# Performance work log

Measured on AMD Instinct MI355X. Metric: run time of the kernel, lower is better.

Reference implementation:

```python
import jax, jax.numpy as jnp
import numpy as np

N, E, G = 50000, 800000, 128
IN, HID, HEAD = 1280, 256, 4
DH = HID // HEAD
EPS = 1e-5
ATT_SCALE = 1.0 / np.sqrt(1280.0).astype(np.float32)  # hardcoded in source


def _seg_softmax(x, seg, n):
    # softmax over segments along axis 0; x: [K] or [K, H]
    m = jax.ops.segment_max(x, seg, num_segments=n)
    e = jnp.exp(x - m[seg])
    s = jax.ops.segment_sum(e, seg, num_segments=n)
    return e / s[seg]


def _bn(x, g, b):
    # eval-mode BatchNorm1d with init running stats (mean=0, var=1)
    return g * x * (1.0 / np.sqrt(1.0 + EPS)) + b


def _ln(x, g, b):
    mu = x.mean(-1, keepdims=True)
    var = ((x - mu) ** 2).mean(-1, keepdims=True)
    return g * (x - mu) / jnp.sqrt(var + EPS) + b


def setup_inputs() -> dict:
    key = jax.random.key(0)
    ks = jax.random.split(key, 40)
    rn = lambda i, shp, s=0.05: jax.random.normal(ks[i], shp, jnp.float32) * s
    inp = {
        "h": jax.random.normal(ks[0], (N, IN), jnp.float32),
        "gcn_w0": rn(1, (IN, HID)), "gcn_b0": rn(2, (HID,), 0.01),
        "gcn_w1": rn(3, (HID, HID)), "gcn_b1": rn(4, (HID,), 0.01),
        "bn_gcn0_g": 1.0 + rn(5, (HID,), 0.1), "bn_gcn0_b": rn(6, (HID,), 0.01),
        "bn_gcn1_g": 1.0 + rn(7, (HID,), 0.1), "bn_gcn1_b": rn(8, (HID,), 0.01),
        "gat_w0": rn(9, (IN, HID)), "gat_al0": rn(10, (HEAD, DH)), "gat_ar0": rn(11, (HEAD, DH)), "gat_bias0": rn(12, (HID,), 0.01),
        "gat_w1": rn(13, (HID, HID)), "gat_al1": rn(14, (HEAD, DH)), "gat_ar1": rn(15, (HEAD, DH)), "gat_bias1": rn(16, (HID,), 0.01),
        "bn_gat0_g": 1.0 + rn(17, (HID,), 0.1), "bn_gat0_b": rn(18, (HID,), 0.01),
        "bn_gat1_g": 1.0 + rn(19, (HID,), 0.1), "bn_gat1_b": rn(20, (HID,), 0.01),
        "gate_w": rn(21, (2 * HID, HID)), "gate_b": rn(22, (HID,), 0.01),
        "qw": rn(23, (HEAD, HID, HID)), "kw": rn(24, (HEAD, HID, HID)), "vw": rn(25, (HEAD, HID, HID)),
        "ct_w": rn(26, (HEAD * HID, HID)),
        "ff_w1": rn(27, (HID, 2 * HID)), "ff_b1": rn(28, (2 * HID,), 0.01),
        "ff_w2": rn(29, (2 * HID, HID)), "ff_b2": rn(30, (HID,), 0.01),
        "ln_g": 1.0 + rn(31, (HID,), 0.1), "ln_b": rn(32, (HID,), 0.01),
        "src": jax.random.randint(ks[33], (E,), 0, N, jnp.int32),
        "dst": jax.random.randint(ks[34], (E,), 0, N, jnp.int32),
        "gid": jnp.sort(jax.random.randint(ks[35], (N,), 0, G, jnp.int32)),
        "num_graphs": G,
    }
    return inp


def reference(h, gcn_w0, gcn_b0, gcn_w1, gcn_b1, bn_gcn0_g, bn_gcn0_b, bn_gcn1_g, bn_gcn1_b,
              gat_w0, gat_al0, gat_ar0, gat_bias0, gat_w1, gat_al1, gat_ar1, gat_bias1,
              bn_gat0_g, bn_gat0_b, bn_gat1_g, bn_gat1_b, gate_w, gate_b,
              qw, kw, vw, ct_w, ff_w1, ff_b1, ff_w2, ff_b2, ln_g, ln_b,
              src, dst, gid, num_graphs):
    n = h.shape[0]
    ones_e = jnp.ones(src.shape[0], h.dtype)
    # dgl.mean_nodes per graph
    cnt = jnp.clip(jax.ops.segment_sum(jnp.ones(n, h.dtype), gid, num_segments=num_graphs), 1.0)
    init_avg_h = jax.ops.segment_sum(h, gid, num_segments=num_graphs) / cnt[:, None]
    # GraphConv norm='both', degrees clamped to >=1
    deg_out = jnp.clip(jax.ops.segment_sum(ones_e, src, num_segments=n), 1.0)
    deg_in = jnp.clip(jax.ops.segment_sum(ones_e, dst, num_segments=n), 1.0)
    ns, nd = deg_out ** -0.5, deg_in ** -0.5

    def gcn(x, w, b):
        m = (x * ns[:, None]) @ w  # [N, HID]
        return jax.ops.segment_sum(m[src], dst, num_segments=n) * nd[:, None] + b

    hg = jax.nn.relu(_bn(gcn(h, gcn_w0, gcn_b0), bn_gcn0_g, bn_gcn0_b))
    hg = jax.nn.relu(_bn(gcn(hg, gcn_w1, gcn_b1), bn_gcn1_g, bn_gcn1_b)) + hg

    def gat(x, w, al, ar, b):
        f = (x @ w).reshape(n, HEAD, DH)
        el = (f * al).sum(-1)  # [N, HEAD]
        er = (f * ar).sum(-1)
        e = jax.nn.leaky_relu(el[src] + er[dst], 0.2)  # [E, HEAD]
        alpha = _seg_softmax(e, dst, n)  # edge softmax over incoming edges
        out = jax.ops.segment_sum(alpha[:, :, None] * f[src], dst, num_segments=n)
        return out.reshape(n, HID) + b

    ha = jax.nn.elu(_bn(gat(h, gat_w0, gat_al0, gat_ar0, gat_bias0), bn_gat0_g, bn_gat0_b))
    ha = jax.nn.elu(_bn(gat(ha, gat_w1, gat_al1, gat_ar1, gat_bias1), bn_gat1_g, bn_gat1_b)) + ha

    gate = jax.nn.sigmoid(jnp.concatenate([hg, ha], axis=1) @ gate_w + gate_b)
    x = gate * hg + (1.0 - gate) * ha  # residue_h

    # transformer_block: per-graph node softmax attention
    q = jnp.einsum('nd,hde->nhe', x, qw)
    k = jnp.einsum('nd,hde->nhe', x, kw)
    v = jnp.einsum('nd,hde->nhe', x, vw)
    att = (q * k).sum(-1) * ATT_SCALE  # [N, HEAD]
    alpha = _seg_softmax(att, gid, num_graphs)  # dgl.softmax_nodes per head
    mo = (v * alpha[:, :, None]).reshape(n, HEAD * HID) @ ct_w
    x1 = _ln(mo + x, ln_g, ln_b)
    x2 = _ln(jax.nn.relu(x1 @ ff_w1 + ff_b1) @ ff_w2 + ff_b2 + x1, ln_g, ln_b)

    readout = jax.ops.segment_sum(x2, gid, num_segments=num_graphs)
    return readout, init_avg_h
```

## Files before the change

### kernel.cpp

```cpp
#include <hip/hip_runtime.h>

#define NN 50000
#define NE 800000
#define NG 128
#define DIN 1280
#define HIDDEN 256
#define BNS 0.9999950000374997f
#define ATT_SCALE 0.027950849718747373f
#define LN_EPS 1e-5f

typedef __attribute__((ext_vector_type(8))) short short8;
typedef __attribute__((ext_vector_type(4))) float floatx4;

__device__ __forceinline__ float b2f(unsigned short u) {
  return __uint_as_float(((unsigned int)u) << 16);
}
__device__ __forceinline__ unsigned short f2b(float f) {
  unsigned int x = __float_as_uint(f);
  x += 0x7fffu + ((x >> 16) & 1u);
  return (unsigned short)(x >> 16);
}

__global__ void transpose_w_k(const float* __restrict__ src, unsigned short* __restrict__ dst,
                              int K, int Nc) {
  int idx = blockIdx.x * 256 + threadIdx.x;
  if (idx >= K * Nc) return;
  int n = idx / K, k = idx % K;
  dst[idx] = f2b(src[(size_t)k * Nc + n]);
}

__global__ void mw_k(const float* __restrict__ qw, const float* __restrict__ kw,
                     unsigned short* __restrict__ dst) {
  int col = blockIdx.x;
  int d = threadIdx.x;
  int hh = col >> 8, dp = col & 255;
  const float* qr = qw + ((size_t)hh * 256 + d) * 256;
  const float* kr = kw + ((size_t)hh * 256 + dp) * 256;
  float s = 0.f;
  for (int e = 0; e < 256; e += 4) {
    float4 a = *(const float4*)(qr + e);
    float4 b = *(const float4*)(kr + e);
    s += a.x * b.x + a.y * b.y + a.z * b.z + a.w * b.w;
  }
  dst[(size_t)col * 256 + d] = f2b(s);
}

__global__ void w2_k(const float* __restrict__ vw, const float* __restrict__ ctw,
                     unsigned short* __restrict__ dst) {
  int b = blockIdx.x;
  int c = threadIdx.x;
  int hh = b >> 8, d = b & 255;
  const float* vr = vw + ((size_t)hh * 256 + d) * 256;
  float s = 0.f;
  for (int e = 0; e < 256; ++e)
    s += vr[e] * ctw[(size_t)(hh * 256 + e) * 256 + c];
  dst[(size_t)c * 1024 + b] = f2b(s);
}

__global__ void cvt_avg_k(const float* __restrict__ h, const int* __restrict__ gid,
                          unsigned short* __restrict__ h_bf, float* __restrict__ out1) {
  int row0 = blockIdx.x * 50;
  int tid = threadIdx.x;
  float acc[5] = {0, 0, 0, 0, 0};
  int cur_g = gid[row0];
  for (int r = 0; r < 50; ++r) {
    int row = row0 + r;
    int g = gid[row];
    if (g != cur_g) {
#pragma unroll
      for (int j = 0; j < 5; ++j) {
        atomicAdd(&out1[(size_t)cur_g * DIN + j * 256 + tid], acc[j]);
        acc[j] = 0.f;
      }
      cur_g = g;
    }
#pragma unroll
    for (int j = 0; j < 5; ++j) {
      float v = h[(size_t)row * DIN + j * 256 + tid];
      acc[j] += v;
      h_bf[(size_t)row * DIN + j * 256 + tid] = f2b(v);
    }
  }
#pragma unroll
  for (int j = 0; j < 5; ++j)
    atomicAdd(&out1[(size_t)cur_g * DIN + j * 256 + tid], acc[j]);
}

__global__ void div_avg_k(const int* __restrict__ start, float* __restrict__ out1) {
  int idx = blockIdx.x * 256 + threadIdx.x;
  if (idx >= NG * DIN) return;
  int g = idx / DIN;
  float cnt = (float)(start[g + 1] - start[g]);
  if (cnt < 1.f) cnt = 1.f;
  out1[idx] /= cnt;
}

__global__ void graph_bounds_k(const int* __restrict__ gid, int* __restrict__ start, int n) {
  int i = blockIdx.x * 256 + threadIdx.x;
  if (i >= n) return;
  int g = gid[i];
  if (i == 0) {
    for (int gg = 0; gg <= g; ++gg) start[gg] = 0;
  } else {
    int gp = gid[i - 1];
    for (int gg = gp + 1; gg <= g; ++gg) start[gg] = i;
  }
  if (i == n - 1) {
    for (int gg = g + 1; gg <= NG; ++gg) start[gg] = n;
  }
}

__global__ void degrees_k(const int* __restrict__ src, const int* __restrict__ dst,
                          int* __restrict__ deg_out, int* __restrict__ deg_in, int e) {
  int i = blockIdx.x * 256 + threadIdx.x;
  if (i >= e) return;
  atomicAdd(&deg_out[src[i]], 1);
  atomicAdd(&deg_in[dst[i]], 1);
}

__global__ void invsqrt_k(const int* __restrict__ deg_out, const int* __restrict__ deg_in,
                          float* __restrict__ ns, float* __restrict__ nd, int n) {
  int i = blockIdx.x * 256 + threadIdx.x;
  if (i >= n) return;
  int a = deg_out[i]; if (a < 1) a = 1;
  int b = deg_in[i];  if (b < 1) b = 1;
  ns[i] = rsqrtf((float)a);
  nd[i] = rsqrtf((float)b);
}

__global__ void scan_local_k(const int* __restrict__ deg, int* __restrict__ row_ptr,
                             int* __restrict__ bsum) {
  __shared__ int buf[256];
  int b = blockIdx.x, t = threadIdx.x;
  int i = b * 256 + t;
  int v = (i < NN) ? deg[i] : 0;
  buf[t] = v;
  __syncthreads();
  for (int off = 1; off < 256; off <<= 1) {
    int tv = (t >= off) ? buf[t - off] : 0;
    __syncthreads();
    buf[t] += tv;
    __syncthreads();
  }
  if (i < NN) row_ptr[i] = buf[t] - v;
  if (t == 255) bsum[b] = buf[255];
}

__global__ void scan_bsum_k(int* __restrict__ bsum, int* __restrict__ boff, int nb,
                            int* __restrict__ row_ptr) {
  __shared__ int buf[256];
  int t = threadIdx.x;
  int v = (t < nb) ? bsum[t] : 0;
  buf[t] = v;
  __syncthreads();
  for (int off = 1; off < 256; off <<= 1) {
    int tv = (t >= off) ? buf[t - off] : 0;
    __syncthreads();
    buf[t] += tv;
    __syncthreads();
  }
  if (t < nb) boff[t] = buf[t] - v;
  if (t == 0) row_ptr[NN] = NE;
}

__global__ void scan_add_k(int* __restrict__ row_ptr, const int* __restrict__ boff) {
  int i = blockIdx.x * 256 + threadIdx.x;
  if (i >= NN) return;
  row_ptr[i] += boff[blockIdx.x];
}

__global__ void fill_csr_k(const int* __restrict__ src, const int* __restrict__ dst,
                           const int* __restrict__ row_ptr, int* __restrict__ fill,
                           int* __restrict__ csr_src, int e) {
  int i = blockIdx.x * 256 + threadIdx.x;
  if (i >= e) return;
  int d = dst[i];
  int pos = row_ptr[d] + atomicAdd(&fill[d], 1);
  csr_src[pos] = src[i];
}

template <int MODE>
__global__ __launch_bounds__(256, 2) void gemm_bf16(const unsigned short* __restrict__ A,
                                                    const unsigned short* __restrict__ Bt,
                                                    void* __restrict__ Cout,
                                                    const float* __restrict__ bias,
                                                    int M, int K, int Nc,
                                                    const unsigned short* __restrict__ xtile,
                                                    float* __restrict__ attp,
                                                    const float* __restrict__ ascale) {
  __shared__ unsigned short sbuf[16384];
  unsigned short* lA = sbuf;
  unsigned short* lB = sbuf + 8192;
  const int tid = threadIdx.x;
  const int n0 = blockIdx.x * 128;
  const int m0 = blockIdx.y * 128;
  const int w = tid >> 6;
  const int lane = tid & 63;
  const int wr = (w >> 1) * 64;
  const int wc = (w & 1) * 64;
  const int quad = lane >> 4;
  const int l15 = lane & 15;
  const int js = tid & 7;
  const int mbase = tid >> 3;
  const int wbase = w * 64;

  floatx4 acc[4][4];
#pragma unroll
  for (int i = 0; i < 4; ++i)
#pragma unroll
    for (int j = 0; j < 4; ++j) acc[i][j] = (floatx4)0.0f;

  for (int k0 = 0; k0 < K; k0 += 64) {
    __syncthreads();
    if (MODE == 6) {
#pragma unroll
      for (int it = 0; it < 4; ++it) {
        int m = it * 32 + mbase;
        int gm = m0 + m;
        if (gm >= M) gm = M - 1;
        uint4 va = *(const uint4*)(A + (size_t)gm * 256 + (k0 & 255) + js * 8);
        float s = ascale[(size_t)gm * 4 + (k0 >> 8)];
        unsigned short* pp = (unsigned short*)&va;
#pragma unroll
        for (int c = 0; c < 8; ++c) pp[c] = f2b(b2f(pp[c]) * s);
        *(uint4*)(lA + (size_t)(m * 8 + (js ^ (m & 7))) * 8) = va;
      }
    } else {
#pragma unroll
      for (int it = 0; it < 4; ++it) {
        int c = it * 256 + wbase + lane;
        int m = c >> 3, g = c & 7;
        int gm = m0 + m;
        if (gm >= M) gm = M - 1;
        const unsigned short* gp = A + (size_t)gm * K + k0 + (g ^ (m & 7)) * 8;
        __builtin_amdgcn_global_load_lds(
            (const __attribute__((address_space(1))) unsigned int*)gp,
            (__attribute__((address_space(3))) unsigned int*)(lA + (size_t)(it * 256 + wbase) * 8),
            16, 0, 0);
      }
    }
#pragma unroll
    for (int it = 0; it < 4; ++it) {
      int c = it * 256 + wbase + lane;
      int m = c >> 3, g = c & 7;
      int gn = n0 + m;
      const unsigned short* gp = Bt + (size_t)gn * K + k0 + (g ^ (m & 7)) * 8;
      __builtin_amdgcn_global_load_lds(
          (const __attribute__((address_space(1))) unsigned int*)gp,
          (__attribute__((address_space(3))) unsigned int*)(lB + (size_t)(it * 256 + wbase) * 8),
          16, 0, 0);
    }
    __syncthreads();
#pragma unroll
    for (int ks = 0; ks < 2; ++ks) {
      int kb = ks * 4 + quad;
      short8 af[4], bfr[4];
#pragma unroll
      for (int ri = 0; ri < 4; ++ri) {
        int r = wr + ri * 16 + l15;
        af[ri] = *(const short8*)(lA + (size_t)(r * 8 + (kb ^ (r & 7))) * 8);
      }
#pragma unroll
      for (int ci = 0; ci < 4; ++ci) {
        int c = wc + ci * 16 + l15;
        bfr[ci] = *(const short8*)(lB + (size_t)(c * 8 + (kb ^ (c & 7))) * 8);
      }
#pragma unroll
      for (int ri = 0; ri < 4; ++ri)
#pragma unroll
        for (int ci = 0; ci < 4; ++ci)
          acc[ri][ci] = __builtin_amdgcn_mfma_f32_16x16x32_bf16(af[ri], bfr[ci], acc[ri][ci], 0, 0, 0);
    }
  }

  if (MODE == 4) {
    __syncthreads();
    int cb = n0 & 255;
#pragma unroll
    for (int it2 = 0; it2 < 8; ++it2) {
      int linear = it2 * 256 + tid;
      int rr = linear >> 4;
      int c8 = (linear & 15) * 8;
      int gr = m0 + rr;
      if (gr >= M) gr = M - 1;
      *(uint4*)(sbuf + rr * 128 + c8) = *(const uint4*)(xtile + (size_t)gr * 256 + cb + c8);
    }
    __syncthreads();
    int head = n0 >> 8;
#pragma unroll
    for (int ri = 0; ri < 4; ++ri) {
      int lrow = wr + ri * 16 + quad * 4;
#pragma unroll
      for (int r = 0; r < 4; ++r) {
        float p = 0.f;
#pragma unroll
        for (int ci = 0; ci < 4; ++ci)
          p += acc[ri][ci][r] * b2f(sbuf[(lrow + r) * 128 + wc + ci * 16 + l15]);
        p += __shfl_xor(p, 1);
        p += __shfl_xor(p, 2);
        p += __shfl_xor(p, 4);
        p += __shfl_xor(p, 8);
        if (l15 == 0) {
          int grow = m0 + lrow + r;
          if (grow < M) atomicAdd(&attp[(size_t)grow * 4 + head], p * ATT_SCALE);
        }
      }
    }
    return;
  }

  if (MODE == 7) {
#pragma unroll
    for (int ri = 0; ri < 4; ++ri) {
      int row = m0 + wr + ri * 16 + quad * 4;
#pragma unroll
      for (int ci = 0; ci < 4; ++ci) {
        int col = n0 + wc + ci * 16 + l15;
        float bv = bias[col];
#pragma unroll
        for (int r = 0; r < 4; ++r) {
          if (row + r < M) {
            float g = 1.f / (1.f + expf(-(acc[ri][ci][r] + bv)));
            float hg = b2f(xtile[(size_t)(row + r) * 512 + col]);
            float ha = b2f(xtile[(size_t)(row + r) * 512 + 256 + col]);
            ((unsigned short*)Cout)[(size_t)(row + r) * Nc + col] = f2b(g * hg + (1.f - g) * ha);
          }
        }
      }
    }
    return;
  }

#pragma unroll
  for (int ri = 0; ri < 4; ++ri) {
    int row = m0 + wr + ri * 16 + quad * 4;
#pragma unroll
    for (int ci = 0; ci < 4; ++ci) {
      int col = n0 + wc + ci * 16 + l15;
      float bv = (MODE == 2) ? bias[col] : 0.f;
#pragma unroll
      for (int r = 0; r < 4; ++r) {
        if (row + r < M) {
          float v = acc[ri][ci][r];
          if (MODE == 2) { v += bv; v = fmaxf(v, 0.f); }
          if (MODE == 1)
            ((float*)Cout)[(size_t)(row + r) * Nc + col] = v;
          else
            ((unsigned short*)Cout)[(size_t)(row + r) * Nc + col] = f2b(v);
        }
      }
    }
  }
}

__global__ void gcn_agg_k(const unsigned short* __restrict__ m, int ldm,
                          const int* __restrict__ row_ptr, const int* __restrict__ csr_src,
                          const float* __restrict__ ns, const float* __restrict__ nd,
                          const float* __restrict__ bias,
                          const float* __restrict__ bng, const float* __restrict__ bnb,
                          const unsigned short* __restrict__ resid, int ldr,
                          unsigned short* __restrict__ out, int ldo) {
  int node = blockIdx.x * 4 + (threadIdx.x >> 6);
  if (node >= NN) return;
  int lane = threadIdx.x & 63;
  int s = row_ptr[node], e = row_ptr[node + 1];
  float a0 = 0, a1 = 0, a2 = 0, a3 = 0;
  for (int i = s; i < e; ++i) {
    int u = csr_src[i];
    float w = ns[u];
    ushort4 v = *(const ushort4*)(m + (size_t)u * ldm + lane * 4);
    a0 += w * b2f(v.x); a1 += w * b2f(v.y); a2 += w * b2f(v.z); a3 += w * b2f(v.w);
  }
  float ndv = nd[node];
  int col = lane * 4;
  float vals[4] = {a0, a1, a2, a3};
  ushort4 o;
#pragma unroll
  for (int c = 0; c < 4; ++c) {
    float v = vals[c] * ndv + bias[col + c];
    v = bng[col + c] * v * BNS + bnb[col + c];
    v = fmaxf(v, 0.f);
    if (resid) v += b2f(resid[(size_t)node * ldr + col + c]);
    ((unsigned short*)&o)[c] = f2b(v);
  }
  *(ushort4*)(out + (size_t)node * ldo + col) = o;
}

__global__ void elr_k(const unsigned short* __restrict__ f, int ldf,
                      const float* __restrict__ al, const float* __restrict__ ar,
                      float* __restrict__ elr) {
  int node = blockIdx.x * 4 + (threadIdx.x >> 6);
  if (node >= NN) return;
  int lane = threadIdx.x & 63;
  int head = lane >> 4;
  int col = lane * 4;
  int dcol = col & 63;
  ushort4 v = *(const ushort4*)(f + (size_t)node * ldf + col);
  float pl = 0, pr = 0;
#pragma unroll
  for (int c = 0; c < 4; ++c) {
    float x = b2f(((unsigned short*)&v)[c]);
    pl += x * al[head * 64 + dcol + c];
    pr += x * ar[head * 64 + dcol + c];
  }
#pragma unroll
  for (int off = 1; off < 16; off <<= 1) {
    pl += __shfl_xor(pl, off);
    pr += __shfl_xor(pr, off);
  }
  if ((lane & 15) == 0) {
    elr[(size_t)node * 8 + head] = pl;
    elr[(size_t)node * 8 + 4 + head] = pr;
  }
}

__global__ void gat_agg_k(const unsigned short* __restrict__ f, int ldf,
                          const int* __restrict__ row_ptr, const int* __restrict__ csr_src,
                          const float* __restrict__ elr,
                          const float* __restrict__ bias,
                          const float* __restrict__ bng, const float* __restrict__ bnb,
                          const unsigned short* __restrict__ resid, int ldr,
                          unsigned short* __restrict__ out, int ldo) {
  int node = blockIdx.x * 4 + (threadIdx.x >> 6);
  if (node >= NN) return;
  int lane = threadIdx.x & 63;
  int s = row_ptr[node], e = row_ptr[node + 1];
  float4 er = *(const float4*)(elr + (size_t)node * 8 + 4);
  float m0 = -1e30f, m1 = -1e30f, m2 = -1e30f, m3 = -1e30f;
  for (int i = s + lane; i < e; i += 64) {
    int u = csr_src[i];
    float4 el = *(const float4*)(elr + (size_t)u * 8);
    float t;
    t = el.x + er.x; t = t > 0.f ? t : 0.2f * t; m0 = fmaxf(m0, t);
    t = el.y + er.y; t = t > 0.f ? t : 0.2f * t; m1 = fmaxf(m1, t);
    t = el.z + er.z; t = t > 0.f ? t : 0.2f * t; m2 = fmaxf(m2, t);
    t = el.w + er.w; t = t > 0.f ? t : 0.2f * t; m3 = fmaxf(m3, t);
  }
#pragma unroll
  for (int off = 1; off < 64; off <<= 1) {
    m0 = fmaxf(m0, __shfl_xor(m0, off));
    m1 = fmaxf(m1, __shfl_xor(m1, off));
    m2 = fmaxf(m2, __shfl_xor(m2, off));
    m3 = fmaxf(m3, __shfl_xor(m3, off));
  }
  float s0 = 0, s1 = 0, s2 = 0, s3 = 0;
  for (int i = s + lane; i < e; i += 64) {
    int u = csr_src[i];
    float4 el = *(const float4*)(elr + (size_t)u * 8);
    float t;
    t = el.x + er.x; t = t > 0.f ? t : 0.2f * t; s0 += expf(t - m0);
    t = el.y + er.y; t = t > 0.f ? t : 0.2f * t; s1 += expf(t - m1);
    t = el.z + er.z; t = t > 0.f ? t : 0.2f * t; s2 += expf(t - m2);
    t = el.w + er.w; t = t > 0.f ? t : 0.2f * t; s3 += expf(t - m3);
  }
#pragma unroll
  for (int off = 1; off < 64; off <<= 1) {
    s0 += __shfl_xor(s0, off);
    s1 += __shfl_xor(s1, off);
    s2 += __shfl_xor(s2, off);
    s3 += __shfl_xor(s3, off);
  }
  int head = lane >> 4;
  float erh = head == 0 ? er.x : head == 1 ? er.y : head == 2 ? er.z : er.w;
  float mh = head == 0 ? m0 : head == 1 ? m1 : head == 2 ? m2 : m3;
  float sh = head == 0 ? s0 : head == 1 ? s1 : head == 2 ? s2 : s3;
  float inv_sh = (sh > 0.f) ? 1.f / sh : 0.f;
  float a0 = 0, a1 = 0, a2 = 0, a3 = 0;
  for (int i = s; i < e; ++i) {
    int u = csr_src[i];
    float t = elr[(size_t)u * 8 + head] + erh;
    t = t > 0.f ? t : 0.2f * t;
    float wgt = expf(t - mh) * inv_sh;
    ushort4 v = *(const ushort4*)(f + (size_t)u * ldf + lane * 4);
    a0 += wgt * b2f(v.x); a1 += wgt * b2f(v.y); a2 += wgt * b2f(v.z); a3 += wgt * b2f(v.w);
  }
  int col = lane * 4;
  float vals[4] = {a0, a1, a2, a3};
  ushort4 o;
#pragma unroll
  for (int c = 0; c < 4; ++c) {
    float v = vals[c] + bias[col + c];
    v = bng[col + c] * v * BNS + bnb[col + c];
    v = (v > 0.f) ? v : (expf(v) - 1.f);
    if (resid) v += b2f(resid[(size_t)node * ldr + col + c]);
    ((unsigned short*)&o)[c] = f2b(v);
  }
  *(ushort4*)(out + (size_t)node * ldo + col) = o;
}

__global__ void gsoftmax_k(const float* __restrict__ att, const int* __restrict__ start,
                           float* __restrict__ alpha) {
  int g = blockIdx.x;
  int s = start[g], e = start[g + 1];
  int tid = threadIdx.x;
  __shared__ float red[256];
  __shared__ float mh[4], sh[4];
  float lm[4] = {-1e30f, -1e30f, -1e30f, -1e30f};
  for (int i = s + tid; i < e; i += 256) {
    float4 a = *(const float4*)(att + (size_t)i * 4);
    lm[0] = fmaxf(lm[0], a.x); lm[1] = fmaxf(lm[1], a.y);
    lm[2] = fmaxf(lm[2], a.z); lm[3] = fmaxf(lm[3], a.w);
  }
#pragma unroll
  for (int h = 0; h < 4; ++h) {
    red[tid] = lm[h]; __syncthreads();
    for (int off = 128; off > 0; off >>= 1) {
      if (tid < off) red[tid] = fmaxf(red[tid], red[tid + off]);
      __syncthreads();
    }
    if (tid == 0) mh[h] = red[0];
    __syncthreads();
  }
  float ls[4] = {0, 0, 0, 0};
  for (int i = s + tid; i < e; i += 256) {
    float4 a = *(const float4*)(att + (size_t)i * 4);
    ls[0] += expf(a.x - mh[0]); ls[1] += expf(a.y - mh[1]);
    ls[2] += expf(a.z - mh[2]); ls[3] += expf(a.w - mh[3]);
  }
#pragma unroll
  for (int h = 0; h < 4; ++h) {
    red[tid] = ls[h]; __syncthreads();
    for (int off = 128; off > 0; off >>= 1) {
      if (tid < off) red[tid] += red[tid + off];
      __syncthreads();
    }
    if (tid == 0) sh[h] = red[0];
    __syncthreads();
  }
  for (int i = s + tid; i < e; i += 256) {
    float4 a = *(const float4*)(att + (size_t)i * 4);
    float4 o;
    o.x = expf(a.x - mh[0]) / sh[0];
    o.y = expf(a.y - mh[1]) / sh[1];
    o.z = expf(a.z - mh[2]) / sh[2];
    o.w = expf(a.w - mh[3]) / sh[3];
    *(float4*)(alpha + (size_t)i * 4) = o;
  }
}

__global__ void ln1_k(const unsigned short* __restrict__ mo, const unsigned short* __restrict__ x,
                      const float* __restrict__ g, const float* __restrict__ b,
                      unsigned short* __restrict__ x1) {
  int node = blockIdx.x * 4 + (threadIdx.x >> 6);
  if (node >= NN) return;
  int lane = threadIdx.x & 63;
  int c = lane * 4;
  ushort4 a = *(const ushort4*)(mo + (size_t)node * HIDDEN + c);
  ushort4 xx = *(const ushort4*)(x + (size_t)node * HIDDEN + c);
  float v0 = b2f(a.x) + b2f(xx.x), v1 = b2f(a.y) + b2f(xx.y);
  float v2 = b2f(a.z) + b2f(xx.z), v3 = b2f(a.w) + b2f(xx.w);
  float sm = v0 + v1 + v2 + v3;
#pragma unroll
  for (int off = 1; off < 64; off <<= 1) sm += __shfl_xor(sm, off);
  float mu = sm * (1.f / 256.f);
  float d0 = v0 - mu, d1 = v1 - mu, d2 = v2 - mu, d3 = v3 - mu;
  float sq = d0 * d0 + d1 * d1 + d2 * d2 + d3 * d3;
#pragma unroll
  for (int off = 1; off < 64; off <<= 1) sq += __shfl_xor(sq, off);
  float inv = rsqrtf(sq * (1.f / 256.f) + LN_EPS);
  ushort4 ob;
  ob.x = f2b(g[c + 0] * d0 * inv + b[c + 0]);
  ob.y = f2b(g[c + 1] * d1 * inv + b[c + 1]);
  ob.z = f2b(g[c + 2] * d2 * inv + b[c + 2]);
  ob.w = f2b(g[c + 3] * d3 * inv + b[c + 3]);
  *(ushort4*)(x1 + (size_t)node * HIDDEN + c) = ob;
}

__global__ void ln2_k(const unsigned short* __restrict__ ff2o, const float* __restrict__ ffb2,
                      const unsigned short* __restrict__ x1,
                      const float* __restrict__ g, const float* __restrict__ b,
                      unsigned short* __restrict__ x2) {
  int node = blockIdx.x * 4 + (threadIdx.x >> 6);
  if (node >= NN) return;
  int lane = threadIdx.x & 63;
  int c = lane * 4;
  ushort4 a = *(const ushort4*)(ff2o + (size_t)node * HIDDEN + c);
  ushort4 xx = *(const ushort4*)(x1 + (size_t)node * HIDDEN + c);
  float v0 = b2f(a.x) + ffb2[c + 0] + b2f(xx.x), v1 = b2f(a.y) + ffb2[c + 1] + b2f(xx.y);
  float v2 = b2f(a.z) + ffb2[c + 2] + b2f(xx.z), v3 = b2f(a.w) + ffb2[c + 3] + b2f(xx.w);
  float sm = v0 + v1 + v2 + v3;
#pragma unroll
  for (int off = 1; off < 64; off <<= 1) sm += __shfl_xor(sm, off);
  float mu = sm * (1.f / 256.f);
  float d0 = v0 - mu, d1 = v1 - mu, d2 = v2 - mu, d3 = v3 - mu;
  float sq = d0 * d0 + d1 * d1 + d2 * d2 + d3 * d3;
#pragma unroll
  for (int off = 1; off < 64; off <<= 1) sq += __shfl_xor(sq, off);
  float inv = rsqrtf(sq * (1.f / 256.f) + LN_EPS);
  ushort4 ob;
  ob.x = f2b(g[c + 0] * d0 * inv + b[c + 0]);
  ob.y = f2b(g[c + 1] * d1 * inv + b[c + 1]);
  ob.z = f2b(g[c + 2] * d2 * inv + b[c + 2]);
  ob.w = f2b(g[c + 3] * d3 * inv + b[c + 3]);
  *(ushort4*)(x2 + (size_t)node * HIDDEN + c) = ob;
}

__global__ void readout_k(const unsigned short* __restrict__ x2, const int* __restrict__ start,
                          float* __restrict__ out0) {
  int g = blockIdx.x;
  int c = threadIdx.x;
  float acc = 0.f;
  for (int i = start[g]; i < start[g + 1]; ++i) acc += b2f(x2[(size_t)i * HIDDEN + c]);
  out0[(size_t)g * HIDDEN + c] = acc;
}

static const size_t OFF_BUFA   = 0;
static const size_t OFF_C01    = 128000000;
static const size_t OFF_HG0    = 179200000;
static const size_t OFF_HA0    = 204800000;
static const size_t OFF_M1     = 230400000;
static const size_t OFF_F1     = 256000000;
static const size_t OFF_XCAT   = 281600000;
static const size_t OFF_GLOGIT = 332800000;
static const size_t OFF_XB     = 358400000;
static const size_t OFF_MO     = 384000000;
static const size_t OFF_X1     = 409600000;
static const size_t OFF_ATT    = 435200000;
static const size_t OFF_ALPHA  = OFF_ATT + 800000;
static const size_t OFF_ELR0   = OFF_ALPHA + 800000;
static const size_t OFF_ELR1   = OFF_ELR0 + 1600000;
static const size_t OFF_START  = OFF_ELR1 + 1600000;
static const size_t OFF_DEGO   = OFF_START + 1024;
static const size_t OFF_DEGI   = OFF_DEGO + 200704;
static const size_t OFF_NS     = OFF_DEGI + 200704;
static const size_t OFF_ND     = OFF_NS + 200704;
static const size_t OFF_ROWP   = OFF_ND + 200704;
static const size_t OFF_FILL   = OFF_ROWP + 200704;
static const size_t OFF_BSUM   = OFF_FILL + 200704;
static const size_t OFF_BOFF   = OFF_BSUM + 1024;
static const size_t OFF_CSRS   = OFF_BOFF + 1024;
static const size_t OFF_W01T   = OFF_CSRS + 3200000;
static const size_t OFF_W1T    = OFF_W01T + 1310720;
static const size_t OFF_W1GT   = OFF_W1T + 131072;
static const size_t OFF_GATEWT = OFF_W1GT + 131072;
static const size_t OFF_WMVT   = OFF_GATEWT + 262144;
static const size_t OFF_CTWT   = OFF_WMVT + 1048576;
static const size_t OFF_FFW1T  = OFF_CTWT + 524288;
static const size_t OFF_FFW2T  = OFF_FFW1T + 262144;
static const size_t WS_NEED    = OFF_FFW2T + 262144;

extern "C" void kernel_launch(void* const* d_in, const int* in_sizes, int n_in,
                              void* d_out, int out_size, void* d_ws, size_t ws_size,
                              hipStream_t stream) {
  if (ws_size < WS_NEED) return;

  const float* h       = (const float*)d_in[0];
  const float* gcn_w0  = (const float*)d_in[1];
  const float* gcn_b0  = (const float*)d_in[2];
  const float* gcn_w1  = (const float*)d_in[3];
  const float* gcn_b1  = (const float*)d_in[4];
  const float* bn_gcn0_g = (const float*)d_in[5];
  const float* bn_gcn0_b = (const float*)d_in[6];
  const float* bn_gcn1_g = (const float*)d_in[7];
  const float* bn_gcn1_b = (const float*)d_in[8];
  const float* gat_w0  = (const float*)d_in[9];
  const float* gat_al0 = (const float*)d_in[10];
  const float* gat_ar0 = (const float*)d_in[11];
  const float* gat_bias0 = (const float*)d_in[12];
  const float* gat_w1  = (const float*)d_in[13];
  const float* gat_al1 = (const float*)d_in[14];
  const float* gat_ar1 = (const float*)d_in[15];
  const float* gat_bias1 = (const float*)d_in[16];
  const float* bn_gat0_g = (const float*)d_in[17];
  const float* bn_gat0_b = (const float*)d_in[18];
  const float* bn_gat1_g = (const float*)d_in[19];
  const float* bn_gat1_b = (const float*)d_in[20];
  const float* gate_w  = (const float*)d_in[21];
  const float* gate_b  = (const float*)d_in[22];
  const float* qw      = (const float*)d_in[23];
  const float* kw      = (const float*)d_in[24];
  const float* vw      = (const float*)d_in[25];
  const float* ct_w    = (const float*)d_in[26];
  const float* ff_w1   = (const float*)d_in[27];
  const float* ff_b1   = (const float*)d_in[28];
  const float* ff_w2   = (const float*)d_in[29];
  const float* ff_b2   = (const float*)d_in[30];
  const float* ln_g    = (const float*)d_in[31];
  const float* ln_b    = (const float*)d_in[32];
  const int* srcv = (const int*)d_in[33];
  const int* dstv = (const int*)d_in[34];
  const int* gid  = (const int*)d_in[35];

  char* ws = (char*)d_ws;
  unsigned short* h_bf = (unsigned short*)(ws + OFF_BUFA);
  unsigned short* ff1o = (unsigned short*)(ws + OFF_BUFA);
  unsigned short* ff2o = (unsigned short*)(ws + OFF_BUFA + 51200000);
  unsigned short* x2   = (unsigned short*)(ws + OFF_BUFA + 76800000);
  unsigned short* c01  = (unsigned short*)(ws + OFF_C01);
  unsigned short* hg0  = (unsigned short*)(ws + OFF_HG0);
  unsigned short* ha0  = (unsigned short*)(ws + OFF_HA0);
  unsigned short* m1   = (unsigned short*)(ws + OFF_M1);
  unsigned short* f1   = (unsigned short*)(ws + OFF_F1);
  unsigned short* xcat = (unsigned short*)(ws + OFF_XCAT);
  unsigned short* xb   = (unsigned short*)(ws + OFF_XB);
  unsigned short* mo   = (unsigned short*)(ws + OFF_MO);
  unsigned short* x1   = (unsigned short*)(ws + OFF_X1);
  float* att           = (float*)(ws + OFF_ATT);
  float* alpha         = (float*)(ws + OFF_ALPHA);
  float* elr0          = (float*)(ws + OFF_ELR0);
  float* elr1          = (float*)(ws + OFF_ELR1);
  int* start   = (int*)(ws + OFF_START);
  int* deg_out = (int*)(ws + OFF_DEGO);
  int* deg_in  = (int*)(ws + OFF_DEGI);
  float* ns    = (float*)(ws + OFF_NS);
  float* nd    = (float*)(ws + OFF_ND);
  int* row_ptr = (int*)(ws + OFF_ROWP);
  int* fill    = (int*)(ws + OFF_FILL);
  int* bsum    = (int*)(ws + OFF_BSUM);
  int* boff    = (int*)(ws + OFF_BOFF);
  int* csr_src = (int*)(ws + OFF_CSRS);
  unsigned short* w01t   = (unsigned short*)(ws + OFF_W01T);
  unsigned short* w1t    = (unsigned short*)(ws + OFF_W1T);
  unsigned short* w1gt   = (unsigned short*)(ws + OFF_W1GT);
  unsigned short* gatewt = (unsigned short*)(ws + OFF_GATEWT);
  unsigned short* wmvt   = (unsigned short*)(ws + OFF_WMVT);
  unsigned short* w2t    = (unsigned short*)(ws + OFF_CTWT);
  unsigned short* ffw1t  = (unsigned short*)(ws + OFF_FFW1T);
  unsigned short* ffw2t  = (unsigned short*)(ws + OFF_FFW2T);

  float* out0 = (float*)d_out;
  float* out1 = out0 + NG * HIDDEN;

  hipMemsetAsync(deg_out, 0, NN * 4, stream);
  hipMemsetAsync(deg_in, 0, NN * 4, stream);
  hipMemsetAsync(fill, 0, NN * 4, stream);
  hipMemsetAsync(out1, 0, NG * DIN * 4, stream);
  hipMemsetAsync(att, 0, NN * 4 * 4, stream);

  transpose_w_k<<<(1280 * 256 + 255) / 256, 256, 0, stream>>>(gcn_w0, w01t, 1280, 256);
  transpose_w_k<<<(1280 * 256 + 255) / 256, 256, 0, stream>>>(gat_w0, w01t + 256 * 1280, 1280, 256);
  transpose_w_k<<<(256 * 256 + 255) / 256, 256, 0, stream>>>(gcn_w1, w1t, 256, 256);
  transpose_w_k<<<(256 * 256 + 255) / 256, 256, 0, stream>>>(gat_w1, w1gt, 256, 256);
  transpose_w_k<<<(512 * 256 + 255) / 256, 256, 0, stream>>>(gate_w, gatewt, 512, 256);
  mw_k<<<1024, 256, 0, stream>>>(qw, kw, wmvt);
  w2_k<<<1024, 256, 0, stream>>>(vw, ct_w, w2t);
  transpose_w_k<<<(256 * 512 + 255) / 256, 256, 0, stream>>>(ff_w1, ffw1t, 256, 512);
  transpose_w_k<<<(512 * 256 + 255) / 256, 256, 0, stream>>>(ff_w2, ffw2t, 512, 256);

  graph_bounds_k<<<(NN + 255) / 256, 256, 0, stream>>>(gid, start, NN);
  degrees_k<<<(NE + 255) / 256, 256, 0, stream>>>(srcv, dstv, deg_out, deg_in, NE);
  invsqrt_k<<<(NN + 255) / 256, 256, 0, stream>>>(deg_out, deg_in, ns, nd, NN);
  const int NB_SCAN = (NN + 255) / 256;
  scan_local_k<<<NB_SCAN, 256, 0, stream>>>(deg_in, row_ptr, bsum);
  scan_bsum_k<<<1, 256, 0, stream>>>(bsum, boff, NB_SCAN, row_ptr);
  scan_add_k<<<NB_SCAN, 256, 0, stream>>>(row_ptr, boff);
  fill_csr_k<<<(NE + 255) / 256, 256, 0, stream>>>(srcv, dstv, row_ptr, fill, csr_src, NE);

  cvt_avg_k<<<NN / 50, 256, 0, stream>>>(h, gid, h_bf, out1);
  div_avg_k<<<(NG * DIN + 255) / 256, 256, 0, stream>>>(start, out1);

  const int MB = (NN + 127) / 128;
  gemm_bf16<0><<<dim3(4, MB), 256, 0, stream>>>(h_bf, w01t, c01, nullptr, NN, 1280, 512,
                                                nullptr, nullptr, nullptr);
  gcn_agg_k<<<NN / 4, 256, 0, stream>>>(c01, 512, row_ptr, csr_src, ns, nd,
                                        gcn_b0, bn_gcn0_g, bn_gcn0_b, nullptr, 0, hg0, 256);
  elr_k<<<NN / 4, 256, 0, stream>>>(c01 + 256, 512, gat_al0, gat_ar0, elr0);
  gat_agg_k<<<NN / 4, 256, 0, stream>>>(c01 + 256, 512, row_ptr, csr_src, elr0,
                                        gat_bias0, bn_gat0_g, bn_gat0_b, nullptr, 0, ha0, 256);
  gemm_bf16<0><<<dim3(2, MB), 256, 0, stream>>>(hg0, w1t, m1, nullptr, NN, 256, 256,
                                                nullptr, nullptr, nullptr);
  gcn_agg_k<<<NN / 4, 256, 0, stream>>>(m1, 256, row_ptr, csr_src, ns, nd,
                                        gcn_b1, bn_gcn1_g, bn_gcn1_b, hg0, 256, xcat, 512);
  gemm_bf16<0><<<dim3(2, MB), 256, 0, stream>>>(ha0, w1gt, f1, nullptr, NN, 256, 256,
                                                nullptr, nullptr, nullptr);
  elr_k<<<NN / 4, 256, 0, stream>>>(f1, 256, gat_al1, gat_ar1, elr1);
  gat_agg_k<<<NN / 4, 256, 0, stream>>>(f1, 256, row_ptr, csr_src, elr1,
                                        gat_bias1, bn_gat1_g, bn_gat1_b, ha0, 256, xcat + 256, 512);
  gemm_bf16<7><<<dim3(2, MB), 256, 0, stream>>>(xcat, gatewt, xb, gate_b, NN, 512, 256,
                                                xcat, nullptr, nullptr);
  gemm_bf16<4><<<dim3(8, MB), 256, 0, stream>>>(xb, wmvt, nullptr, nullptr, NN, 256, 1024,
                                                xb, att, nullptr);
  gsoftmax_k<<<NG, 256, 0, stream>>>(att, start, alpha);
  gemm_bf16<6><<<dim3(2, MB), 256, 0, stream>>>(xb, w2t, mo, nullptr, NN, 1024, 256,
                                                nullptr, nullptr, alpha);
  ln1_k<<<NN / 4, 256, 0, stream>>>(mo, xb, ln_g, ln_b, x1);
  gemm_bf16<2><<<dim3(4, MB), 256, 0, stream>>>(x1, ffw1t, ff1o, ff_b1, NN, 256, 512,
                                                nullptr, nullptr, nullptr);
  gemm_bf16<0><<<dim3(2, MB), 256, 0, stream>>>(ff1o, ffw2t, ff2o, nullptr, NN, 512, 256,
                                                nullptr, nullptr, nullptr);
  ln2_k<<<NN / 4, 256, 0, stream>>>(ff2o, ff_b2, x1, ln_g, ln_b, x2);
  readout_k<<<NG, 256, 0, stream>>>(x2, start, out0);
}
```

Measured before the change: 1.664 ms.

## Double-buffer GEMM LDS, fuse GAT el/er into GEMM, batch layer-1 GEMMs, fuse readout

The GEMM main loop now double-buffers its LDS tiles so the next K-tile's global-to-LDS loads overlap the current MFMA work. GAT attention logits (el/er) are computed in the GEMM epilogue, which removes the separate elr kernels. The two layer-1 GEMMs are batched into one launch using gridDim.z with fixed pointer offsets. The readout is fused into ln2 through per-node atomics, and cvt_avg is vectorised to float4 loads. LDS use doubles to 64KB per block, which may cut occupancy, and the per-node atomics into 128 graphs could contend.

Measured after the change: 1.830 ms. +9.9%, slower.

```diff
diff --git a/kernel.cpp b/kernel.cpp
--- a/kernel.cpp
+++ b/kernel.cpp
@@ -61,29 +61,30 @@
                           unsigned short* __restrict__ h_bf, float* __restrict__ out1) {
   int row0 = blockIdx.x * 50;
   int tid = threadIdx.x;
-  float acc[5] = {0, 0, 0, 0, 0};
+  float4 acc = {0.f, 0.f, 0.f, 0.f};
   int cur_g = gid[row0];
+  int c4 = tid * 4;
   for (int r = 0; r < 50; ++r) {
     int row = row0 + r;
     int g = gid[row];
     if (g != cur_g) {
-#pragma unroll
-      for (int j = 0; j < 5; ++j) {
-        atomicAdd(&out1[(size_t)cur_g * DIN + j * 256 + tid], acc[j]);
-        acc[j] = 0.f;
-      }
+      atomicAdd(&out1[(size_t)cur_g * DIN + c4 + 0], acc.x);
+      atomicAdd(&out1[(size_t)cur_g * DIN + c4 + 1], acc.y);
+      atomicAdd(&out1[(size_t)cur_g * DIN + c4 + 2], acc.z);
+      atomicAdd(&out1[(size_t)cur_g * DIN + c4 + 3], acc.w);
+      acc = {0.f, 0.f, 0.f, 0.f};
       cur_g = g;
     }
-#pragma unroll
-    for (int j = 0; j < 5; ++j) {
-      float v = h[(size_t)row * DIN + j * 256 + tid];
-      acc[j] += v;
-      h_bf[(size_t)row * DIN + j * 256 + tid] = f2b(v);
-    }
-  }
-#pragma unroll
-  for (int j = 0; j < 5; ++j)
-    atomicAdd(&out1[(size_t)cur_g * DIN + j * 256 + tid], acc[j]);
+    float4 v = *(const float4*)(h + (size_t)row * DIN + c4);
+    acc.x += v.x; acc.y += v.y; acc.z += v.z; acc.w += v.w;
+    ushort4 o;
+    o.x = f2b(v.x); o.y = f2b(v.y); o.z = f2b(v.z); o.w = f2b(v.w);
+    *(ushort4*)(h_bf + (size_t)row * DIN + c4) = o;
+  }
+  atomicAdd(&out1[(size_t)cur_g * DIN + c4 + 0], acc.x);
+  atomicAdd(&out1[(size_t)cur_g * DIN + c4 + 1], acc.y);
+  atomicAdd(&out1[(size_t)cur_g * DIN + c4 + 2], acc.z);
+  atomicAdd(&out1[(size_t)cur_g * DIN + c4 + 3], acc.w);
 }
 
 __global__ void div_avg_k(const int* __restrict__ start, float* __restrict__ out1) {
@@ -187,10 +188,12 @@
                                                     int M, int K, int Nc,
                                                     const unsigned short* __restrict__ xtile,
                                                     float* __restrict__ attp,
-                                                    const float* __restrict__ ascale) {
-  __shared__ unsigned short sbuf[16384];
-  unsigned short* lA = sbuf;
-  unsigned short* lB = sbuf + 8192;
+                                                    const float* __restrict__ ascale,
+                                                    const float* __restrict__ al,
+                                                    const float* __restrict__ ar,
+                                                    float* __restrict__ elr,
+                                                    int ecol0) {
+  __shared__ unsigned short sbuf[32768];
   const int tid = threadIdx.x;
   const int n0 = blockIdx.x * 128;
   const int m0 = blockIdx.y * 128;
@@ -204,77 +207,138 @@
   const int mbase = tid >> 3;
   const int wbase = w * 64;
 
+  bool do_elr = (MODE == 8);
+  const unsigned short* Ap = A;
+  const unsigned short* Bp = Bt;
+  unsigned short* Cp = (unsigned short*)Cout;
+  if (MODE == 8 && gridDim.z == 2) {
+    if (blockIdx.z == 0) {
+      do_elr = false;
+    } else {
+      Ap += 12800000;
+      Bp += 65536;
+      Cp += 12800000;
+    }
+  }
+
   floatx4 acc[4][4];
 #pragma unroll
   for (int i = 0; i < 4; ++i)
 #pragma unroll
     for (int j = 0; j < 4; ++j) acc[i][j] = (floatx4)0.0f;
 
-  for (int k0 = 0; k0 < K; k0 += 64) {
-    __syncthreads();
-    if (MODE == 6) {
+  if constexpr (MODE == 6) {
+    unsigned short* lA = sbuf;
+    unsigned short* lB = sbuf + 8192;
+    for (int k0 = 0; k0 < K; k0 += 64) {
+      __syncthreads();
 #pragma unroll
       for (int it = 0; it < 4; ++it) {
         int m = it * 32 + mbase;
         int gm = m0 + m;
         if (gm >= M) gm = M - 1;
-        uint4 va = *(const uint4*)(A + (size_t)gm * 256 + (k0 & 255) + js * 8);
+        uint4 va = *(const uint4*)(Ap + (size_t)gm * 256 + (k0 & 255) + js * 8);
         float s = ascale[(size_t)gm * 4 + (k0 >> 8)];
         unsigned short* pp = (unsigned short*)&va;
 #pragma unroll
         for (int c = 0; c < 8; ++c) pp[c] = f2b(b2f(pp[c]) * s);
         *(uint4*)(lA + (size_t)(m * 8 + (js ^ (m & 7))) * 8) = va;
       }
-    } else {
+#pragma unroll
+      for (int it = 0; it < 4; ++it) {
+        int c = it * 256 + wbase + lane;
+        int m = c >> 3, g = c & 7;
+        int gn = n0 + m;
+        const unsigned short* gp = Bp + (size_t)gn * K + k0 + (g ^ (m & 7)) * 8;
+        __builtin_amdgcn_global_load_lds(
+            (const __attribute__((address_space(1))) unsigned int*)gp,
+            (__attribute__((address_space(3))) unsigned int*)(lB + (size_t)(it * 256 + wbase) * 8),
+            16, 0, 0);
+      }
+      __syncthreads();
+#pragma unroll
+      for (int ks = 0; ks < 2; ++ks) {
+        int kb = ks * 4 + quad;
+        short8 af[4], bfr[4];
+#pragma unroll
+        for (int ri = 0; ri < 4; ++ri) {
+          int r = wr + ri * 16 + l15;
+          af[ri] = *(const short8*)(lA + (size_t)(r * 8 + (kb ^ (r & 7))) * 8);
+        }
+#pragma unroll
+        for (int ci = 0; ci < 4; ++ci) {
+          int c = wc + ci * 16 + l15;
+          bfr[ci] = *(const short8*)(lB + (size_t)(c * 8 + (kb ^ (c & 7))) * 8);
+        }
+#pragma unroll
+        for (int ri = 0; ri < 4; ++ri)
+#pragma unroll
+          for (int ci = 0; ci < 4; ++ci)
+            acc[ri][ci] = __builtin_amdgcn_mfma_f32_16x16x32_bf16(af[ri], bfr[ci], acc[ri][ci], 0, 0, 0);
+      }
+    }
+    __syncthreads();
+  } else {
+    const int nt = K >> 6;
+    auto stage = [&](int b, int k0) {
+      unsigned short* lA = sbuf + b * 16384;
+      unsigned short* lB = lA + 8192;
 #pragma unroll
       for (int it = 0; it < 4; ++it) {
         int c = it * 256 + wbase + lane;
         int m = c >> 3, g = c & 7;
         int gm = m0 + m;
         if (gm >= M) gm = M - 1;
-        const unsigned short* gp = A + (size_t)gm * K + k0 + (g ^ (m & 7)) * 8;
+        const unsigned short* gp = Ap + (size_t)gm * K + k0 + (g ^ (m & 7)) * 8;
         __builtin_amdgcn_global_load_lds(
             (const __attribute__((address_space(1))) unsigned int*)gp,
             (__attribute__((address_space(3))) unsigned int*)(lA + (size_t)(it * 256 + wbase) * 8),
             16, 0, 0);
       }
-    }
-#pragma unroll
-    for (int it = 0; it < 4; ++it) {
-      int c = it * 256 + wbase + lane;
-      int m = c >> 3, g = c & 7;
-      int gn = n0 + m;
-      const unsigned short* gp = Bt + (size_t)gn * K + k0 + (g ^ (m & 7)) * 8;
-      __builtin_amdgcn_global_load_lds(
-          (const __attribute__((address_space(1))) unsigned int*)gp,
-          (__attribute__((address_space(3))) unsigned int*)(lB + (size_t)(it * 256 + wbase) * 8),
-          16, 0, 0);
-    }
+#pragma unroll
+      for (int it = 0; it < 4; ++it) {
+        int c = it * 256 + wbase + lane;
+        int m = c >> 3, g = c & 7;
+        int gn = n0 + m;
+        const unsigned short* gp = Bp + (size_t)gn * K + k0 + (g ^ (m & 7)) * 8;
+        __builtin_amdgcn_global_load_lds(
+            (const __attribute__((address_space(1))) unsigned int*)gp,
+            (__attribute__((address_space(3))) unsigned int*)(lB + (size_t)(it * 256 + wbase) * 8),
+            16, 0, 0);
+      }
+    };
+    stage(0, 0);
     __syncthreads();
-#pragma unroll
-    for (int ks = 0; ks < 2; ++ks) {
-      int kb = ks * 4 + quad;
-      short8 af[4], bfr[4];
-#pragma unroll
-      for (int ri = 0; ri < 4; ++ri) {
-        int r = wr + ri * 16 + l15;
-        af[ri] = *(const short8*)(lA + (size_t)(r * 8 + (kb ^ (r & 7))) * 8);
-      }
-#pragma unroll
-      for (int ci = 0; ci < 4; ++ci) {
-        int c = wc + ci * 16 + l15;
-        bfr[ci] = *(const short8*)(lB + (size_t)(c * 8 + (kb ^ (c & 7))) * 8);
-      }
-#pragma unroll
-      for (int ri = 0; ri < 4; ++ri)
-#pragma unroll
-        for (int ci = 0; ci < 4; ++ci)
-          acc[ri][ci] = __builtin_amdgcn_mfma_f32_16x16x32_bf16(af[ri], bfr[ci], acc[ri][ci], 0, 0, 0);
+    for (int t = 0; t < nt; ++t) {
+      int cur = t & 1;
+      if (t + 1 < nt) stage(cur ^ 1, (t + 1) * 64);
+      unsigned short* lA = sbuf + cur * 16384;
+      unsigned short* lB = lA + 8192;
+#pragma unroll
+      for (int ks = 0; ks < 2; ++ks) {
+        int kb = ks * 4 + quad;
+        short8 af[4], bfr[4];
+#pragma unroll
+        for (int ri = 0; ri < 4; ++ri) {
+          int r = wr + ri * 16 + l15;
+          af[ri] = *(const short8*)(lA + (size_t)(r * 8 + (kb ^ (r & 7))) * 8);
+        }
+#pragma unroll
+        for (int ci = 0; ci < 4; ++ci) {
+          int c = wc + ci * 16 + l15;
+          bfr[ci] = *(const short8*)(lB + (size_t)(c * 8 + (kb ^ (c & 7))) * 8);
+        }
+#pragma unroll
+        for (int ri = 0; ri < 4; ++ri)
+#pragma unroll
+          for (int ci = 0; ci < 4; ++ci)
+            acc[ri][ci] = __builtin_amdgcn_mfma_f32_16x16x32_bf16(af[ri], bfr[ci], acc[ri][ci], 0, 0, 0);
+      }
+      __syncthreads();
     }
   }
 
   if (MODE == 4) {
-    __syncthreads();
     int cb = n0 & 255;
 #pragma unroll
     for (int it2 = 0; it2 < 8; ++it2) {
@@ -323,12 +387,41 @@
             float g = 1.f / (1.f + expf(-(acc[ri][ci][r] + bv)));
             float hg = b2f(xtile[(size_t)(row + r) * 512 + col]);
             float ha = b2f(xtile[(size_t)(row + r) * 512 + 256 + col]);
-            ((unsigned short*)Cout)[(size_t)(row + r) * Nc + col] = f2b(g * hg + (1.f - g) * ha);
+            Cp[(size_t)(row + r) * Nc + col] = f2b(g * hg + (1.f - g) * ha);
           }
         }
       }
     }
     return;
+  }
+
+  if (MODE == 8 && do_elr && n0 >= ecol0) {
+    int head = (n0 - ecol0 + wc) >> 6;
+#pragma unroll
+    for (int ri = 0; ri < 4; ++ri) {
+      int lrow = wr + ri * 16 + quad * 4;
+#pragma unroll
+      for (int r = 0; r < 4; ++r) {
+        float pl = 0.f, pr = 0.f;
+#pragma unroll
+        for (int ci = 0; ci < 4; ++ci) {
+          float fv = acc[ri][ci][r];
+          pl += fv * al[head * 64 + ci * 16 + l15];
+          pr += fv * ar[head * 64 + ci * 16 + l15];
+        }
+        pl += __shfl_xor(pl, 1); pl += __shfl_xor(pl, 2);
+        pl += __shfl_xor(pl, 4); pl += __shfl_xor(pl, 8);
+        pr += __shfl_xor(pr, 1); pr += __shfl_xor(pr, 2);
+        pr += __shfl_xor(pr, 4); pr += __shfl_xor(pr, 8);
+        if (l15 == 0) {
+          int grow = m0 + lrow + r;
+          if (grow < M) {
+            elr[(size_t)grow * 8 + head] = pl;
+            elr[(size_t)grow * 8 + 4 + head] = pr;
+          }
+        }
+      }
+    }
   }
 
 #pragma unroll
@@ -346,7 +439,7 @@
           if (MODE == 1)
             ((float*)Cout)[(size_t)(row + r) * Nc + col] = v;
           else
-            ((unsigned short*)Cout)[(size_t)(row + r) * Nc + col] = f2b(v);
+            Cp[(size_t)(row + r) * Nc + col] = f2b(v);
         }
       }
     }
@@ -384,34 +477,6 @@
     ((unsigned short*)&o)[c] = f2b(v);
   }
   *(ushort4*)(out + (size_t)node * ldo + col) = o;
-}
-
-__global__ void elr_k(const unsigned short* __restrict__ f, int ldf,
-                      const float* __restrict__ al, const float* __restrict__ ar,
-                      float* __restrict__ elr) {
-  int node = blockIdx.x * 4 + (threadIdx.x >> 6);
-  if (node >= NN) return;
-  int lane = threadIdx.x & 63;
-  int head = lane >> 4;
-  int col = lane * 4;
-  int dcol = col & 63;
-  ushort4 v = *(const ushort4*)(f + (size_t)node * ldf + col);
-  float pl = 0, pr = 0;
-#pragma unroll
-  for (int c = 0; c < 4; ++c) {
-    float x = b2f(((unsigned short*)&v)[c]);
-    pl += x * al[head * 64 + dcol + c];
-    pr += x * ar[head * 64 + dcol + c];
-  }
-#pragma unroll
-  for (int off = 1; off < 16; off <<= 1) {
-    pl += __shfl_xor(pl, off);
-    pr += __shfl_xor(pr, off);
-  }
-  if ((lane & 15) == 0) {
-    elr[(size_t)node * 8 + head] = pl;
-    elr[(size_t)node * 8 + 4 + head] = pr;
-  }
 }
 
 __global__ void gat_agg_k(const unsigned short* __restrict__ f, int ldf,
@@ -569,7 +634,7 @@
 __global__ void ln2_k(const unsigned short* __restrict__ ff2o, const float* __restrict__ ffb2,
                       const unsigned short* __restrict__ x1,
                       const float* __restrict__ g, const float* __restrict__ b,
-                      unsigned short* __restrict__ x2) {
+                      const int* __restrict__ gid, float* __restrict__ out0) {
   int node = blockIdx.x * 4 + (threadIdx.x >> 6);
   if (node >= NN) return;
   int lane = threadIdx.x & 63;
@@ -587,21 +652,15 @@
 #pragma unroll
   for (int off = 1; off < 64; off <<= 1) sq += __shfl_xor(sq, off);
   float inv = rsqrtf(sq * (1.f / 256.f) + LN_EPS);
-  ushort4 ob;
-  ob.x = f2b(g[c + 0] * d0 * inv + b[c + 0]);
-  ob.y = f2b(g[c + 1] * d1 * inv + b[c + 1]);
-  ob.z = f2b(g[c + 2] * d2 * inv + b[c + 2]);
-  ob.w = f2b(g[c + 3] * d3 * inv + b[c + 3]);
-  *(ushort4*)(x2 + (size_t)node * HIDDEN + c) = ob;
-}
-
-__global__ void readout_k(const unsigned short* __restrict__ x2, const int* __restrict__ start,
-                          float* __restrict__ out0) {
-  int g = blockIdx.x;
-  int c = threadIdx.x;
-  float acc = 0.f;
-  for (int i = start[g]; i < start[g + 1]; ++i) acc += b2f(x2[(size_t)i * HIDDEN + c]);
-  out0[(size_t)g * HIDDEN + c] = acc;
+  int gg = gid[node];
+  float r0 = b2f(f2b(g[c + 0] * d0 * inv + b[c + 0]));
+  float r1 = b2f(f2b(g[c + 1] * d1 * inv + b[c + 1]));
+  float r2 = b2f(f2b(g[c + 2] * d2 * inv + b[c + 2]));
+  float r3 = b2f(f2b(g[c + 3] * d3 * inv + b[c + 3]));
+  atomicAdd(&out0[(size_t)gg * HIDDEN + c + 0], r0);
+  atomicAdd(&out0[(size_t)gg * HIDDEN + c + 1], r1);
+  atomicAdd(&out0[(size_t)gg * HIDDEN + c + 2], r2);
+  atomicAdd(&out0[(size_t)gg * HIDDEN + c + 3], r3);
 }
 
 static const size_t OFF_BUFA   = 0;
@@ -685,7 +744,6 @@
   unsigned short* h_bf = (unsigned short*)(ws + OFF_BUFA);
   unsigned short* ff1o = (unsigned short*)(ws + OFF_BUFA);
   unsigned short* ff2o = (unsigned short*)(ws + OFF_BUFA + 51200000);
-  unsigned short* x2   = (unsigned short*)(ws + OFF_BUFA + 76800000);
   unsigned short* c01  = (unsigned short*)(ws + OFF_C01);
   unsigned short* hg0  = (unsigned short*)(ws + OFF_HG0);
   unsigned short* ha0  = (unsigned short*)(ws + OFF_HA0);
@@ -724,6 +782,7 @@
   hipMemsetAsync(deg_out, 0, NN * 4, stream);
   hipMemsetAsync(deg_in, 0, NN * 4, stream);
   hipMemsetAsync(fill, 0, NN * 4, stream);
+  hipMemsetAsync(out0, 0, NG * HIDDEN * 4, stream);
   hipMemsetAsync(out1, 0, NG * DIN * 4, stream);
   hipMemsetAsync(att, 0, NN * 4 * 4, stream);
 
@@ -746,38 +805,40 @@
   scan_add_k<<<NB_SCAN, 256, 0, stream>>>(row_ptr, boff);
   fill_csr_k<<<(NE + 255) / 256, 256, 0, stream>>>(srcv, dstv, row_ptr, fill, csr_src, NE);
 
-  cvt_avg_k<<<NN / 50, 256, 0, stream>>>(h, gid, h_bf, out1);
+  cvt_avg_k<<<NN / 50, 320, 0, stream>>>(h, gid, h_bf, out1);
   div_avg_k<<<(NG * DIN + 255) / 256, 256, 0, stream>>>(start, out1);
 
   const int MB = (NN + 127) / 128;
-  gemm_bf16<0><<<dim3(4, MB), 256, 0, stream>>>(h_bf, w01t, c01, nullptr, NN, 1280, 512,
-                                                nullptr, nullptr, nullptr);
+  gemm_bf16<8><<<dim3(4, MB), 256, 0, stream>>>(h_bf, w01t, c01, nullptr, NN, 1280, 512,
+                                                nullptr, nullptr, nullptr,
+                                                gat_al0, gat_ar0, elr0, 256);
   gcn_agg_k<<<NN / 4, 256, 0, stream>>>(c01, 512, row_ptr, csr_src, ns, nd,
                                         gcn_b0, bn_gcn0_g, bn_gcn0_b, nullptr, 0, hg0, 256);
-  elr_k<<<NN / 4, 256, 0, stream>>>(c01 + 256, 512, gat_al0, gat_ar0, elr0);
   gat_agg_k<<<NN / 4, 256, 0, stream>>>(c01 + 256, 512, row_ptr, csr_src, elr0,
                                         gat_bias0, bn_gat0_g, bn_gat0_b, nullptr, 0, ha0, 256);
-  gemm_bf16<0><<<dim3(2, MB), 256, 0, stream>>>(hg0, w1t, m1, nullptr, NN, 256, 256,
-                                                nullptr, nullptr, nullptr);
+  gemm_bf16<8><<<dim3(2, MB, 2), 256, 0, stream>>>(hg0, w1t, m1, nullptr, NN, 256, 256,
+                                                   nullptr, nullptr, nullptr,
+                                                   gat_al1, gat_ar1, elr1, 0);
   gcn_agg_k<<<NN / 4, 256, 0, stream>>>(m1, 256, row_ptr, csr_src, ns, nd,
                                         gcn_b1, bn_gcn1_g, bn_gcn1_b, hg0, 256, xcat, 512);
-  gemm_bf16<0><<<dim3(2, MB), 256, 0, stream>>>(ha0, w1gt, f1, nullptr, NN, 256, 256,
-                                                nullptr, nullptr, nullptr);
-  elr_k<<<NN / 4, 256, 0, stream>>>(f1, 256, gat_al1, gat_ar1, elr1);
   gat_agg_k<<<NN / 4, 256, 0, stream>>>(f1, 256, row_ptr, csr_src, elr1,
                                         gat_bias1, bn_gat1_g, bn_gat1_b, ha0, 256, xcat + 256, 512);
   gemm_bf16<7><<<dim3(2, MB), 256, 0, stream>>>(xcat, gatewt, xb, gate_b, NN, 512, 256,
-                                                xcat, nullptr, nullptr);
+                                                xcat, nullptr, nullptr,
+                                                nullptr, nullptr, nullptr, 0);
   gemm_bf16<4><<<dim3(8, MB), 256, 0, stream>>>(xb, wmvt, nullptr, nullptr, NN, 256, 1024,
-                                                xb, att, nullptr);
+                                                xb, att, nullptr,
+                                                nullptr, nullptr, nullptr, 0);
   gsoftmax_k<<<NG, 256, 0, stream>>>(att, start, alpha);
   gemm_bf16<6><<<dim3(2, MB), 256, 0, stream>>>(xb, w2t, mo, nullptr, NN, 1024, 256,
-                                                nullptr, nullptr, alpha);
+                                                nullptr, nullptr, alpha,
+                                                nullptr, nullptr, nullptr, 0);
   ln1_k<<<NN / 4, 256, 0, stream>>>(mo, xb, ln_g, ln_b, x1);
   gemm_bf16<2><<<dim3(4, MB), 256, 0, stream>>>(x1, ffw1t, ff1o, ff_b1, NN, 256, 512,
-                                                nullptr, nullptr, nullptr);
+                                                nullptr, nullptr, nullptr,
+                                                nullptr, nullptr, nullptr, 0);
   gemm_bf16<0><<<dim3(2, MB), 256, 0, stream>>>(ff1o, ffw2t, ff2o, nullptr, NN, 512, 256,
-                                                nullptr, nullptr, nullptr);
-  ln2_k<<<NN / 4, 256, 0, stream>>>(ff2o, ff_b2, x1, ln_g, ln_b, x2);
-  readout_k<<<NG, 256, 0, stream>>>(x2, start, out0);
-}
+                                                nullptr, nullptr, nullptr,
+                                                nullptr, nullptr, nullptr, 0);
+  ln2_k<<<NN / 4, 256, 0, stream>>>(ff2o, ff_b2, x1, ln_g, ln_b, gid, out0);
+}
```
